# Optimization experiments

Hardware: AMD Instinct MI355X
Metric: run time of the kernel (lower is better)

## Reference

```python
import jax, jax.numpy as jnp
import numpy as np

NEG_SLOPE = 0.2  # PyG GATConv default leaky_relu slope
N_NODES, IN_DIM, HID, HEADS, OUT = 50000, 128, 64, 4, 128
N_EDGES = 800000


def gat_conv(x, src, dst, num_nodes, W, a_src, a_dst, bias, concat):
    """One PyG-style GATConv (add_self_loops already applied to src/dst)."""
    H, C = a_src.shape
    xp = (x @ W).reshape(num_nodes, H, C)            # (N,H,C)
    s = jnp.einsum('nhc,hc->nh', xp, a_src)          # per-node src score
    d = jnp.einsum('nhc,hc->nh', xp, a_dst)          # per-node dst score
    e = s[src] + d[dst]                              # (E,H)
    e = jnp.where(e > 0, e, NEG_SLOPE * e)           # leaky_relu
    # segment softmax over edges grouped by destination node
    m = jax.ops.segment_max(e, dst, num_segments=num_nodes)
    p = jnp.exp(e - m[dst])
    z = jax.ops.segment_sum(p, dst, num_segments=num_nodes)
    alpha = p / (z[dst] + 1e-16)                     # (E,H)
    # scatter-aggregate messages
    out = jax.ops.segment_sum(xp[src] * alpha[:, :, None], dst, num_segments=num_nodes)
    out = out.reshape(num_nodes, H * C) if concat else out.mean(axis=1)
    return out + bias


def setup_inputs() -> dict:
    key = jax.random.key(0)
    ks = jax.random.split(key, 16)
    HC = HEADS * HID
    inp = {
        'x': jax.random.normal(ks[0], (N_NODES, IN_DIM), dtype=jnp.float32),
        'edge_index': jax.random.randint(ks[1], (2, N_EDGES), 0, N_NODES, dtype=jnp.int32),
        'W0': jax.random.normal(ks[2], (IN_DIM, HC), dtype=jnp.float32) * 0.08,
        'a_src0': jax.random.normal(ks[3], (HEADS, HID), dtype=jnp.float32) * 0.1,
        'a_dst0': jax.random.normal(ks[4], (HEADS, HID), dtype=jnp.float32) * 0.1,
        'b0': jnp.zeros((HC,), dtype=jnp.float32),
        'W1': jax.random.normal(ks[5], (HC, HC), dtype=jnp.float32) * 0.06,
        'a_src1': jax.random.normal(ks[6], (HEADS, HID), dtype=jnp.float32) * 0.1,
        'a_dst1': jax.random.normal(ks[7], (HEADS, HID), dtype=jnp.float32) * 0.1,
        'b1': jnp.zeros((HC,), dtype=jnp.float32),
        'W2': jax.random.normal(ks[8], (HC, OUT), dtype=jnp.float32) * 0.06,
        'a_src2': jax.random.normal(ks[9], (1, OUT), dtype=jnp.float32) * 0.1,
        'a_dst2': jax.random.normal(ks[10], (1, OUT), dtype=jnp.float32) * 0.1,
        'b2': jnp.zeros((OUT,), dtype=jnp.float32),
    }
    return inp


def reference(x, edge_index, W0, a_src0, a_dst0, b0, W1, a_src1, a_dst1, b1, W2, a_src2, a_dst2, b2):
    N = x.shape[0]
    loops = jnp.arange(N, dtype=edge_index.dtype)  # add_self_loops=True
    src = jnp.concatenate([edge_index[0], loops])
    dst = jnp.concatenate([edge_index[1], loops])
    h = gat_conv(x, src, dst, N, W0, a_src0, a_dst0, b0, True)
    h = jax.nn.elu(h)
    h = gat_conv(h, src, dst, N, W1, a_src1, a_dst1, b1, True)
    h = jax.nn.elu(h)
    h = gat_conv(h, src, dst, N, W2, a_src2, a_dst2, b2, False)
    return h
```

## Files before the change

### kernel.cpp

```cpp
#include <hip/hip_runtime.h>
#include <hip/hip_bf16.h>
#include <hip/hip_fp16.h>
#include <math.h>

#define N_NODES 50000
#define N_EDGES 800000
#define ET      (N_EDGES + N_NODES)
#define IN_DIM  128
#define HEADS   4
#define HID     64
#define HC      256
#define OUTD    128

typedef _Float16 half8 __attribute__((ext_vector_type(8)));
typedef float f32x4 __attribute__((ext_vector_type(4)));


__global__ void scan1_k(const int* __restrict__ counts, int* __restrict__ offs,
                        int* __restrict__ bsums) {
    __shared__ int sm[512];
    int tid = threadIdx.x;
    int i = blockIdx.x * 512 + tid;
    int v = (i < N_NODES) ? counts[i] : 0;
    sm[tid] = v;
    __syncthreads();
    #pragma unroll
    for (int o = 1; o < 512; o <<= 1) {
        int add = (tid >= o) ? sm[tid - o] : 0;
        __syncthreads();
        sm[tid] += add;
        __syncthreads();
    }
    if (i < N_NODES) offs[i] = sm[tid] - v;
    if (tid == 511) bsums[blockIdx.x] = sm[511];
}

__global__ void scan3_k(int* __restrict__ offs, const int* __restrict__ bsums) {
    __shared__ int base_sm;
    int tid = threadIdx.x;
    if (tid < 64) {
        int p = 0;
        for (int j = tid; j < (int)blockIdx.x; j += 64) p += bsums[j];
        #pragma unroll
        for (int o = 1; o < 64; o <<= 1) p += __shfl_xor(p, o, 64);
        if (tid == 0) base_sm = p;
    }
    __syncthreads();
    int i = blockIdx.x * 512 + tid;
    if (i < N_NODES) offs[i] += base_sm;
    if (i == 0) offs[N_NODES] = ET;
}

__global__ void fill_k(const int* __restrict__ ei, const int* __restrict__ offs,
                       int* __restrict__ counts, int* __restrict__ csr) {
    int i = blockIdx.x * blockDim.x + threadIdx.x;
    if (i >= ET) return;
    int sv, dv;
    if (i < N_EDGES) { sv = ei[i]; dv = ei[N_EDGES + i]; }
    else             { sv = dv = i - N_EDGES; }
    int pos = offs[dv] + atomicSub(&counts[dv], 1) - 1;
    csr[pos] = sv;
}


#define J_HIST  ET
#define J_CVT   (N_NODES * IN_DIM / 4)
#define J_W     131072
#define SETUP_TOTAL (J_HIST + J_CVT + J_W + 2 * N_NODES)

__global__ void setup_k(const int* __restrict__ ei, int* __restrict__ counts,
                        const float* __restrict__ x, __half* __restrict__ xh,
                        const float* __restrict__ W0, __half* __restrict__ Wt0,
                        const float* __restrict__ W1, __half* __restrict__ Wt1,
                        const float* __restrict__ W2, __half* __restrict__ Wt2,
                        float* __restrict__ S2, float* __restrict__ D2) {
    int g = blockIdx.x * 256 + threadIdx.x;
    if (g < J_HIST) {
        int dv = (g < N_EDGES) ? ei[N_EDGES + g] : (g - N_EDGES);
        atomicAdd(&counts[dv], 1);
        return;
    }
    g -= J_HIST;
    if (g < J_CVT) {
        float4 v = *(const float4*)(x + (size_t)g * 4);
        union { __half2 h2[2]; float2 f2; } u;
        u.h2[0] = __floats2half2_rn(v.x, v.y);
        u.h2[1] = __floats2half2_rn(v.z, v.w);
        *(float2*)(xh + (size_t)g * 4) = u.f2;
        return;
    }
    g -= J_CVT;
    if (g < J_W) {
        if (g < 32768) {
            int n = g / IN_DIM, k = g - n * IN_DIM;
            Wt0[g] = __float2half(W0[(size_t)k * HC + n]);
        } else if (g < 98304) {
            int i = g - 32768;
            int n = i / HC, k = i - n * HC;
            Wt1[i] = __float2half(W1[(size_t)k * HC + n]);
        } else {
            int i = g - 98304;
            int n = i / HC, k = i - n * HC;
            Wt2[i] = __float2half(W2[(size_t)k * OUTD + n]);
        }
        return;
    }
    g -= J_W;
    if (g < N_NODES) { S2[g] = 0.f; return; }
    g -= N_NODES;
    if (g < N_NODES) D2[g] = 0.f;
}


__device__ __forceinline__ void async_copy16(void* lds_base, const void* gaddr) {
    __builtin_amdgcn_global_load_lds(
        (const __attribute__((address_space(1))) unsigned int*)gaddr,
        (__attribute__((address_space(3))) unsigned int*)lds_base,
        16, 0, 0);
}

#define CPAD 132

template<int H, int CD, bool ATOMIC>
__global__ __launch_bounds__(256) void gemm_mfma_k(const __half* __restrict__ A,
                                                   const __half* __restrict__ Wt,
                                                   __half* __restrict__ C,
                                                   const float* __restrict__ asrc,
                                                   const float* __restrict__ adst,
                                                   float* __restrict__ S,
                                                   float* __restrict__ D,
                                                   int M, int K, int N) {
    __shared__ __attribute__((aligned(16))) __half smem[128 * CPAD];
    __half* Ah = smem;
    __half* Bh = smem + 128 * 64;
    const int t = threadIdx.x;
    const int w = t >> 6;
    const int lane = t & 63;
    const int wm = w >> 1, wn = w & 1;
    const int cc = lane & 15;
    const int quad = lane >> 4;
    const int row0 = blockIdx.x * 128;
    const int col0 = blockIdx.y * 128;

    f32x4 acc[4][4];
    #pragma unroll
    for (int i = 0; i < 4; ++i)
        #pragma unroll
        for (int j = 0; j < 4; ++j) acc[i][j] = (f32x4){0.f, 0.f, 0.f, 0.f};

    const int srow = lane >> 3;
    const int skq  = (lane & 7) * 8;

    for (int k0 = 0; k0 < K; k0 += 64) {
        __syncthreads();
        #pragma unroll
        for (int hh = 0; hh < 4; ++hh) {
            int ra = row0 + w * 32 + hh * 8 + srow;
            if (ra > M - 1) ra = M - 1;
            async_copy16(&Ah[(w * 32 + hh * 8) * 64],
                         A + (size_t)ra * K + k0 + skq);
            int rb = col0 + w * 32 + hh * 8 + srow;
            async_copy16(&Bh[(w * 32 + hh * 8) * 64],
                         Wt + (size_t)rb * K + k0 + skq);
        }
        __syncthreads();
        #pragma unroll
        for (int c = 0; c < 2; ++c) {
            half8 a[4], b[4];
            #pragma unroll
            for (int i = 0; i < 4; ++i)
                a[i] = *(const half8*)&Ah[(wm * 64 + i * 16 + cc) * 64 + c * 32 + quad * 8];
            #pragma unroll
            for (int j = 0; j < 4; ++j)
                b[j] = *(const half8*)&Bh[(wn * 64 + j * 16 + cc) * 64 + c * 32 + quad * 8];
            #pragma unroll
            for (int i = 0; i < 4; ++i)
                #pragma unroll
                for (int j = 0; j < 4; ++j)
                    acc[i][j] = __builtin_amdgcn_mfma_f32_16x16x32_f16(b[j], a[i], acc[i][j], 0, 0, 0);
        }
    }

    const int hh_ = ATOMIC ? 0 : (blockIdx.y * 2 + wn);
    float4 asj[4], adj[4];
    #pragma unroll
    for (int j = 0; j < 4; ++j) {
        int cb = (ATOMIC ? wn * 64 : 0) + j * 16 + quad * 4;
        asj[j] = *(const float4*)&asrc[hh_ * CD + cb];
        adj[j] = *(const float4*)&adst[hh_ * CD + cb];
    }
    #pragma unroll
    for (int i = 0; i < 4; ++i) {
        float sv = 0.f, dv = 0.f;
        #pragma unroll
        for (int j = 0; j < 4; ++j) {
            sv = fmaf(acc[i][j][0], asj[j].x, sv); dv = fmaf(acc[i][j][0], adj[j].x, dv);
            sv = fmaf(acc[i][j][1], asj[j].y, sv); dv = fmaf(acc[i][j][1], adj[j].y, dv);
            sv = fmaf(acc[i][j][2], asj[j].z, sv); dv = fmaf(acc[i][j][2], adj[j].z, dv);
            sv = fmaf(acc[i][j][3], asj[j].w, sv); dv = fmaf(acc[i][j][3], adj[j].w, dv);
        }
        sv += __shfl_xor(sv, 16, 64); dv += __shfl_xor(dv, 16, 64);
        sv += __shfl_xor(sv, 32, 64); dv += __shfl_xor(dv, 32, 64);
        int r = row0 + wm * 64 + i * 16 + cc;
        if (quad == 0 && r < M) {
            if constexpr (ATOMIC) {
                atomicAdd(&S[r], sv);
                atomicAdd(&D[r], dv);
            } else {
                S[(size_t)r * H + hh_] = sv;
                D[(size_t)r * H + hh_] = dv;
            }
        }
    }

    __syncthreads();
    #pragma unroll
    for (int i = 0; i < 4; ++i) {
        int tr = wm * 64 + i * 16 + cc;
        #pragma unroll
        for (int j = 0; j < 4; ++j) {
            int tc = wn * 64 + j * 16 + quad * 4;
            union { __half2 h2[2]; uint2 u2; } pk;
            pk.h2[0] = __floats2half2_rn(acc[i][j][0], acc[i][j][1]);
            pk.h2[1] = __floats2half2_rn(acc[i][j][2], acc[i][j][3]);
            *(uint2*)&smem[tr * CPAD + tc] = pk.u2;
        }
    }
    __syncthreads();
    #pragma unroll
    for (int rr = 0; rr < 8; ++rr) {
        int r = rr * 16 + (t >> 4);
        int ccol = (t & 15) * 8;
        uint4 v = *(const uint4*)&smem[r * CPAD + ccol];
        int gr = row0 + r;
        if (gr < M)
            *(uint4*)&C[(size_t)gr * N + col0 + ccol] = v;
    }
}


template<int H, int C, bool ELU_OUT, typename OT>
__global__ __launch_bounds__(256) void aggr_k(const __half* __restrict__ xp,
                                              const float* __restrict__ s,
                                              const float* __restrict__ d,
                                              const int* __restrict__ offs,
                                              const int* __restrict__ csr,
                                              const float* __restrict__ bias,
                                              OT* __restrict__ out) {
    constexpr int HCl = H * C;
    constexpr int FPL = HCl / 32;
    constexpr int U = 8;
    const int tid = threadIdx.x;
    const int lane = tid & 63;
    const int l = lane & 31;
    const int par = lane >> 5;
    int wid = blockIdx.x * 4 + (tid >> 6);
    if (wid >= N_NODES) return;
    const int h = (l * FPL) / C;
    const int loff = l * FPL;

    float dh = d[wid * H + h];
    float z = 0.f;
    float acc[FPL];
    #pragma unroll
    for (int k = 0; k < FPL; ++k) acc[k] = 0.f;

    const int e0 = offs[wid];
    const int e1 = offs[wid + 1];

    for (int j = e0; j < e1; j += U) {
        int ss[4];
        #pragma unroll
        for (int k2 = 0; k2 < 4; ++k2) {
            int idx = j + 2 * k2 + par;
            ss[k2] = csr[idx < e1 ? idx : e1 - 1];
        }
        float ev[4];
        #pragma unroll
        for (int k2 = 0; k2 < 4; ++k2)
            ev[k2] = s[ss[k2] * H + h];
        uint4 r4[4];
        uint2 r2[4];
        #pragma unroll
        for (int k2 = 0; k2 < 4; ++k2) {
            const __half* rowp = xp + (size_t)ss[k2] * HCl + loff;
            if constexpr (FPL == 8) r4[k2] = *(const uint4*)rowp;
            else                    r2[k2] = *(const uint2*)rowp;
        }
        #pragma unroll
        for (int k2 = 0; k2 < 4; ++k2) {
            float e = (j + 2 * k2 + par < e1) ? (ev[k2] + dh) : -1e30f;
            e = fmaxf(e, 0.2f * e);
            float pw = __expf(e);
            z += pw;
            if constexpr (FPL == 8) {
                union { uint4 u; __half2 h2[4]; } rr; rr.u = r4[k2];
                #pragma unroll
                for (int q = 0; q < 4; ++q) {
                    acc[2*q]   = fmaf(pw, __half2float(__low2half(rr.h2[q])),  acc[2*q]);
                    acc[2*q+1] = fmaf(pw, __half2float(__high2half(rr.h2[q])), acc[2*q+1]);
                }
            } else {
                union { uint2 u; __half2 h2[2]; } rr; rr.u = r2[k2];
                #pragma unroll
                for (int q = 0; q < 2; ++q) {
                    acc[2*q]   = fmaf(pw, __half2float(__low2half(rr.h2[q])),  acc[2*q]);
                    acc[2*q+1] = fmaf(pw, __half2float(__high2half(rr.h2[q])), acc[2*q+1]);
                }
            }
        }
    }

    z += __shfl_xor(z, 32, 64);
    #pragma unroll
    for (int k = 0; k < FPL; ++k) acc[k] += __shfl_xor(acc[k], 32, 64);

    if (lane >= 32) return;

    float inv = 1.f / (z + 1e-16f);
    float o[FPL];
    #pragma unroll
    for (int k = 0; k < FPL; ++k) {
        o[k] = acc[k] * inv + bias[loff + k];
        if constexpr (ELU_OUT) o[k] = (o[k] > 0.f) ? o[k] : (__expf(o[k]) - 1.f);
    }
    if constexpr (sizeof(OT) == 2 && FPL == 8) {
        union { __half2 h2[4]; uint4 u4; } u;
        u.h2[0] = __floats2half2_rn(o[0], o[1]);
        u.h2[1] = __floats2half2_rn(o[2], o[3]);
        u.h2[2] = __floats2half2_rn(o[4], o[5]);
        u.h2[3] = __floats2half2_rn(o[6], o[7]);
        *(uint4*)((__half*)out + (size_t)wid * HCl + loff) = u.u4;
    } else if constexpr (sizeof(OT) == 4 && FPL == 4) {
        float4 v; v.x = o[0]; v.y = o[1]; v.z = o[2]; v.w = o[3];
        *(float4*)((float*)out + (size_t)wid * HCl + loff) = v;
    } else {
        #pragma unroll
        for (int k = 0; k < FPL; ++k)
            out[(size_t)wid * HCl + loff + k] = (OT)o[k];
    }
}


extern "C" void kernel_launch(void* const* d_in, const int* in_sizes, int n_in,
                              void* d_out, int out_size, void* d_ws, size_t ws_size,
                              hipStream_t stream) {
    const float* x      = (const float*)d_in[0];
    const int*   ei     = (const int*)  d_in[1];
    const float* W0     = (const float*)d_in[2];
    const float* as0    = (const float*)d_in[3];
    const float* ad0    = (const float*)d_in[4];
    const float* b0     = (const float*)d_in[5];
    const float* W1     = (const float*)d_in[6];
    const float* as1    = (const float*)d_in[7];
    const float* ad1    = (const float*)d_in[8];
    const float* b1     = (const float*)d_in[9];
    const float* W2     = (const float*)d_in[10];
    const float* as2    = (const float*)d_in[11];
    const float* ad2    = (const float*)d_in[12];
    const float* b2     = (const float*)d_in[13];
    float* out = (float*)d_out;

    char* p = (char*)d_ws;
    auto take = [&](size_t bytes) {
        char* r = p;
        p += (bytes + 255) & ~(size_t)255;
        return r;
    };
    __half* XPh   = (__half*)take((size_t)N_NODES * HC * 2);
    __half* Hbuf  = (__half*)take((size_t)N_NODES * HC * 2);
    __half* xh    = (__half*)take((size_t)N_NODES * IN_DIM * 2);
    __half* Wt0   = (__half*)take((size_t)IN_DIM * HC * 2);
    __half* Wt1   = (__half*)take((size_t)HC * HC * 2);
    __half* Wt2   = (__half*)take((size_t)HC * OUTD * 2);
    float*  S     = (float*) take((size_t)N_NODES * HEADS * 4);
    float*  D     = (float*) take((size_t)N_NODES * HEADS * 4);
    float*  S2    = (float*) take((size_t)N_NODES * 4);
    float*  D2    = (float*) take((size_t)N_NODES * 4);
    int*    counts= (int*)   take((size_t)N_NODES * 4);
    int*    offs  = (int*)   take((size_t)(N_NODES + 1) * 4);
    int*    bsums = (int*)   take(512 * 4);
    int*    csr   = (int*)   take((size_t)ET * 4);

    const int NB_SCAN = (N_NODES + 511) / 512;
    const int ET_BLOCKS = (ET + 255) / 256;
    const int NODE_BLOCKS = (N_NODES + 3) / 4;
    const int MB = (N_NODES + 127) / 128;
    dim3 g0(MB, HC / 128);
    dim3 g2(MB, OUTD / 128);

    hipMemsetAsync(counts, 0, (size_t)N_NODES * 4, stream);
    setup_k<<<(SETUP_TOTAL + 255) / 256, 256, 0, stream>>>(
        ei, counts, x, xh, W0, Wt0, W1, Wt1, W2, Wt2, S2, D2);

    scan1_k<<<NB_SCAN, 512, 0, stream>>>(counts, offs, bsums);
    scan3_k<<<NB_SCAN, 512, 0, stream>>>(offs, bsums);
    fill_k<<<ET_BLOCKS, 256, 0, stream>>>(ei, offs, counts, csr);

    gemm_mfma_k<HEADS, HID, false><<<g0, 256, 0, stream>>>(xh, Wt0, XPh, as0, ad0, S, D, N_NODES, IN_DIM, HC);
    aggr_k<HEADS, HID, true, __half><<<NODE_BLOCKS, 256, 0, stream>>>(XPh, S, D, offs, csr, b0, Hbuf);

    gemm_mfma_k<HEADS, HID, false><<<g0, 256, 0, stream>>>(Hbuf, Wt1, XPh, as1, ad1, S, D, N_NODES, HC, HC);
    aggr_k<HEADS, HID, true, __half><<<NODE_BLOCKS, 256, 0, stream>>>(XPh, S, D, offs, csr, b1, Hbuf);

    gemm_mfma_k<1, OUTD, true><<<g2, 256, 0, stream>>>(Hbuf, Wt2, XPh, as2, ad2, S2, D2, N_NODES, HC, OUTD);
    aggr_k<1, OUTD, false, float><<<NODE_BLOCKS, 256, 0, stream>>>(XPh, S2, D2, offs, csr, b2, out);
}
```

Before: 388.8 us.

## Persistent double-buffered GEMM with direct B loads and 16-bit CSR indices

The MFMA GEMM becomes a persistent kernel. Each block loops over several M tiles and double-buffers A tiles in LDS, prefetching the next tile or K-chunk while computing the current one. B fragments are now read straight from global memory instead of being staged in LDS, and the output is written directly from registers rather than through an LDS transpose. The CSR neighbour array is narrowed to unsigned short to halve index traffic in the aggregation kernels, but node ids up to 49999 fit in 16 bits only because N is below 65536.

```diff
diff --git a/kernel.cpp b/kernel.cpp
--- a/kernel.cpp
+++ b/kernel.cpp
@@ -52,14 +52,14 @@
 }
 
 __global__ void fill_k(const int* __restrict__ ei, const int* __restrict__ offs,
-                       int* __restrict__ counts, int* __restrict__ csr) {
+                       int* __restrict__ counts, unsigned short* __restrict__ csr) {
     int i = blockIdx.x * blockDim.x + threadIdx.x;
     if (i >= ET) return;
     int sv, dv;
     if (i < N_EDGES) { sv = ei[i]; dv = ei[N_EDGES + i]; }
     else             { sv = dv = i - N_EDGES; }
     int pos = offs[dv] + atomicSub(&counts[dv], 1) - 1;
-    csr[pos] = sv;
+    csr[pos] = (unsigned short)sv;
 }
 
 
@@ -119,67 +119,40 @@
         16, 0, 0);
 }
 
-#define CPAD 132
-
-template<int H, int CD, bool ATOMIC>
-__global__ __launch_bounds__(256) void gemm_mfma_k(const __half* __restrict__ A,
-                                                   const __half* __restrict__ Wt,
-                                                   __half* __restrict__ C,
-                                                   const float* __restrict__ asrc,
-                                                   const float* __restrict__ adst,
-                                                   float* __restrict__ S,
-                                                   float* __restrict__ D,
-                                                   int M, int K, int N) {
-    __shared__ __attribute__((aligned(16))) __half smem[128 * CPAD];
-    __half* Ah = smem;
-    __half* Bh = smem + 128 * 64;
+template<int H, int CD, bool ATOMIC, int KK>
+__global__ __launch_bounds__(256, 3) void gemm_mfma_k(const __half* __restrict__ A,
+                                                      const __half* __restrict__ Wt,
+                                                      __half* __restrict__ C,
+                                                      const float* __restrict__ asrc,
+                                                      const float* __restrict__ adst,
+                                                      float* __restrict__ S,
+                                                      float* __restrict__ D,
+                                                      int M, int N) {
+    constexpr int KC = KK / 64;
+    __shared__ __attribute__((aligned(16))) __half Ah[2][128 * 64];
     const int t = threadIdx.x;
     const int w = t >> 6;
     const int lane = t & 63;
     const int wm = w >> 1, wn = w & 1;
     const int cc = lane & 15;
     const int quad = lane >> 4;
-    const int row0 = blockIdx.x * 128;
     const int col0 = blockIdx.y * 128;
-
-    f32x4 acc[4][4];
-    #pragma unroll
-    for (int i = 0; i < 4; ++i)
-        #pragma unroll
-        for (int j = 0; j < 4; ++j) acc[i][j] = (f32x4){0.f, 0.f, 0.f, 0.f};
-
     const int srow = lane >> 3;
     const int skq  = (lane & 7) * 8;
-
-    for (int k0 = 0; k0 < K; k0 += 64) {
-        __syncthreads();
+    const int MBt = (M + 127) >> 7;
+    const int PB = gridDim.x;
+
+    if ((int)blockIdx.x >= MBt) return;
+
+    auto stage = [&](int mt, int kc, int b) {
         #pragma unroll
         for (int hh = 0; hh < 4; ++hh) {
-            int ra = row0 + w * 32 + hh * 8 + srow;
+            int ra = mt * 128 + w * 32 + hh * 8 + srow;
             if (ra > M - 1) ra = M - 1;
-            async_copy16(&Ah[(w * 32 + hh * 8) * 64],
-                         A + (size_t)ra * K + k0 + skq);
-            int rb = col0 + w * 32 + hh * 8 + srow;
-            async_copy16(&Bh[(w * 32 + hh * 8) * 64],
-                         Wt + (size_t)rb * K + k0 + skq);
-        }
-        __syncthreads();
-        #pragma unroll
-        for (int c = 0; c < 2; ++c) {
-            half8 a[4], b[4];
-            #pragma unroll
-            for (int i = 0; i < 4; ++i)
-                a[i] = *(const half8*)&Ah[(wm * 64 + i * 16 + cc) * 64 + c * 32 + quad * 8];
-            #pragma unroll
-            for (int j = 0; j < 4; ++j)
-                b[j] = *(const half8*)&Bh[(wn * 64 + j * 16 + cc) * 64 + c * 32 + quad * 8];
-            #pragma unroll
-            for (int i = 0; i < 4; ++i)
-                #pragma unroll
-                for (int j = 0; j < 4; ++j)
-                    acc[i][j] = __builtin_amdgcn_mfma_f32_16x16x32_f16(b[j], a[i], acc[i][j], 0, 0, 0);
-        }
-    }
+            async_copy16(&Ah[b][(w * 32 + hh * 8) * 64],
+                         A + (size_t)ra * KK + kc * 64 + skq);
+        }
+    };
 
     const int hh_ = ATOMIC ? 0 : (blockIdx.y * 2 + wn);
     float4 asj[4], adj[4];
@@ -189,52 +162,85 @@
         asj[j] = *(const float4*)&asrc[hh_ * CD + cb];
         adj[j] = *(const float4*)&adst[hh_ * CD + cb];
     }
-    #pragma unroll
-    for (int i = 0; i < 4; ++i) {
-        float sv = 0.f, dv = 0.f;
-        #pragma unroll
-        for (int j = 0; j < 4; ++j) {
-            sv = fmaf(acc[i][j][0], asj[j].x, sv); dv = fmaf(acc[i][j][0], adj[j].x, dv);
-            sv = fmaf(acc[i][j][1], asj[j].y, sv); dv = fmaf(acc[i][j][1], adj[j].y, dv);
-            sv = fmaf(acc[i][j][2], asj[j].z, sv); dv = fmaf(acc[i][j][2], adj[j].z, dv);
-            sv = fmaf(acc[i][j][3], asj[j].w, sv); dv = fmaf(acc[i][j][3], adj[j].w, dv);
-        }
-        sv += __shfl_xor(sv, 16, 64); dv += __shfl_xor(dv, 16, 64);
-        sv += __shfl_xor(sv, 32, 64); dv += __shfl_xor(dv, 32, 64);
-        int r = row0 + wm * 64 + i * 16 + cc;
-        if (quad == 0 && r < M) {
-            if constexpr (ATOMIC) {
-                atomicAdd(&S[r], sv);
-                atomicAdd(&D[r], dv);
-            } else {
-                S[(size_t)r * H + hh_] = sv;
-                D[(size_t)r * H + hh_] = dv;
+
+    int buf = 0;
+    stage(blockIdx.x, 0, 0);
+    asm volatile("s_waitcnt vmcnt(0)" ::: "memory");
+    __builtin_amdgcn_s_barrier();
+
+    for (int mt = blockIdx.x; mt < MBt; mt += PB) {
+        f32x4 acc[4][4];
+        #pragma unroll
+        for (int i = 0; i < 4; ++i)
+            #pragma unroll
+            for (int j = 0; j < 4; ++j) acc[i][j] = (f32x4){0.f, 0.f, 0.f, 0.f};
+
+        #pragma unroll
+        for (int kc = 0; kc < KC; ++kc) {
+            int nmt = mt, nkc = kc + 1;
+            if (nkc == KC) { nmt = mt + PB; nkc = 0; }
+            if (nmt < MBt) stage(nmt, nkc, buf ^ 1);
+
+            #pragma unroll
+            for (int c = 0; c < 2; ++c) {
+                half8 a[4], b[4];
+                #pragma unroll
+                for (int j = 0; j < 4; ++j)
+                    b[j] = *(const half8*)&Wt[(size_t)(col0 + wn * 64 + j * 16 + cc) * KK
+                                              + kc * 64 + c * 32 + quad * 8];
+                #pragma unroll
+                for (int i = 0; i < 4; ++i)
+                    a[i] = *(const half8*)&Ah[buf][(wm * 64 + i * 16 + cc) * 64 + c * 32 + quad * 8];
+                #pragma unroll
+                for (int i = 0; i < 4; ++i)
+                    #pragma unroll
+                    for (int j = 0; j < 4; ++j)
+                        acc[i][j] = __builtin_amdgcn_mfma_f32_16x16x32_f16(b[j], a[i], acc[i][j], 0, 0, 0);
             }
-        }
-    }
-
-    __syncthreads();
-    #pragma unroll
-    for (int i = 0; i < 4; ++i) {
-        int tr = wm * 64 + i * 16 + cc;
-        #pragma unroll
-        for (int j = 0; j < 4; ++j) {
-            int tc = wn * 64 + j * 16 + quad * 4;
-            union { __half2 h2[2]; uint2 u2; } pk;
-            pk.h2[0] = __floats2half2_rn(acc[i][j][0], acc[i][j][1]);
-            pk.h2[1] = __floats2half2_rn(acc[i][j][2], acc[i][j][3]);
-            *(uint2*)&smem[tr * CPAD + tc] = pk.u2;
-        }
-    }
-    __syncthreads();
-    #pragma unroll
-    for (int rr = 0; rr < 8; ++rr) {
-        int r = rr * 16 + (t >> 4);
-        int ccol = (t & 15) * 8;
-        uint4 v = *(const uint4*)&smem[r * CPAD + ccol];
-        int gr = row0 + r;
-        if (gr < M)
-            *(uint4*)&C[(size_t)gr * N + col0 + ccol] = v;
+
+            asm volatile("s_waitcnt vmcnt(0)" ::: "memory");
+            __builtin_amdgcn_s_barrier();
+            __builtin_amdgcn_sched_barrier(0);
+            buf ^= 1;
+        }
+
+        #pragma unroll
+        for (int i = 0; i < 4; ++i) {
+            float sv = 0.f, dv = 0.f;
+            #pragma unroll
+            for (int j = 0; j < 4; ++j) {
+                sv = fmaf(acc[i][j][0], asj[j].x, sv); dv = fmaf(acc[i][j][0], adj[j].x, dv);
+                sv = fmaf(acc[i][j][1], asj[j].y, sv); dv = fmaf(acc[i][j][1], adj[j].y, dv);
+                sv = fmaf(acc[i][j][2], asj[j].z, sv); dv = fmaf(acc[i][j][2], adj[j].z, dv);
+                sv = fmaf(acc[i][j][3], asj[j].w, sv); dv = fmaf(acc[i][j][3], adj[j].w, dv);
+            }
+            sv += __shfl_xor(sv, 16, 64); dv += __shfl_xor(dv, 16, 64);
+            sv += __shfl_xor(sv, 32, 64); dv += __shfl_xor(dv, 32, 64);
+            int r = mt * 128 + wm * 64 + i * 16 + cc;
+            if (quad == 0 && r < M) {
+                if constexpr (ATOMIC) {
+                    atomicAdd(&S[r], sv);
+                    atomicAdd(&D[r], dv);
+                } else {
+                    S[(size_t)r * H + hh_] = sv;
+                    D[(size_t)r * H + hh_] = dv;
+                }
+            }
+        }
+
+        #pragma unroll
+        for (int i = 0; i < 4; ++i) {
+            int gr = mt * 128 + wm * 64 + i * 16 + cc;
+            if (gr >= M) continue;
+            #pragma unroll
+            for (int j = 0; j < 4; ++j) {
+                int tc = col0 + wn * 64 + j * 16 + quad * 4;
+                union { __half2 h2[2]; uint2 u2; } pk;
+                pk.h2[0] = __floats2half2_rn(acc[i][j][0], acc[i][j][1]);
+                pk.h2[1] = __floats2half2_rn(acc[i][j][2], acc[i][j][3]);
+                *(uint2*)&C[(size_t)gr * N + tc] = pk.u2;
+            }
+        }
     }
 }
 
@@ -244,7 +250,7 @@
                                               const float* __restrict__ s,
                                               const float* __restrict__ d,
                                               const int* __restrict__ offs,
-                                              const int* __restrict__ csr,
+                                              const unsigned short* __restrict__ csr,
                                               const float* __restrict__ bias,
                                               OT* __restrict__ out) {
     constexpr int HCl = H * C;
@@ -380,13 +386,13 @@
     int*    counts= (int*)   take((size_t)N_NODES * 4);
     int*    offs  = (int*)   take((size_t)(N_NODES + 1) * 4);
     int*    bsums = (int*)   take(512 * 4);
-    int*    csr   = (int*)   take((size_t)ET * 4);
+    unsigned short* csr = (unsigned short*)take((size_t)ET * 2);
 
     const int NB_SCAN = (N_NODES + 511) / 512;
     const int ET_BLOCKS = (ET + 255) / 256;
     const int NODE_BLOCKS = (N_NODES + 3) / 4;
     const int MB = (N_NODES + 127) / 128;
-    dim3 g0(MB, HC / 128);
+    dim3 g0(MB < 384 ? MB : 384, HC / 128);
     dim3 g2(MB, OUTD / 128);
 
     hipMemsetAsync(counts, 0, (size_t)N_NODES * 4, stream);
@@ -397,12 +403,12 @@
     scan3_k<<<NB_SCAN, 512, 0, stream>>>(offs, bsums);
     fill_k<<<ET_BLOCKS, 256, 0, stream>>>(ei, offs, counts, csr);
 
-    gemm_mfma_k<HEADS, HID, false><<<g0, 256, 0, stream>>>(xh, Wt0, XPh, as0, ad0, S, D, N_NODES, IN_DIM, HC);
+    gemm_mfma_k<HEADS, HID, false, IN_DIM><<<g0, 256, 0, stream>>>(xh, Wt0, XPh, as0, ad0, S, D, N_NODES, HC);
     aggr_k<HEADS, HID, true, __half><<<NODE_BLOCKS, 256, 0, stream>>>(XPh, S, D, offs, csr, b0, Hbuf);
 
-    gemm_mfma_k<HEADS, HID, false><<<g0, 256, 0, stream>>>(Hbuf, Wt1, XPh, as1, ad1, S, D, N_NODES, HC, HC);
+    gemm_mfma_k<HEADS, HID, false, HC><<<g0, 256, 0, stream>>>(Hbuf, Wt1, XPh, as1, ad1, S, D, N_NODES, HC);
     aggr_k<HEADS, HID, true, __half><<<NODE_BLOCKS, 256, 0, stream>>>(XPh, S, D, offs, csr, b1, Hbuf);
 
-    gemm_mfma_k<1, OUTD, true><<<g2, 256, 0, stream>>>(Hbuf, Wt2, XPh, as2, ad2, S2, D2, N_NODES, HC, OUTD);
+    gemm_mfma_k<1, OUTD, true, HC><<<g2, 256, 0, stream>>>(Hbuf, Wt2, XPh, as2, ad2, S2, D2, N_NODES, OUTD);
     aggr_k<1, OUTD, false, float><<<NODE_BLOCKS, 256, 0, stream>>>(XPh, S2, D2, offs, csr, b2, out);
 }
```

Result: slower. 425.6 us (+9.5%).

## Fuse CSR scan and fill into one kernel with in-kernel spin-wait barrier

Applied to the files above, without the earlier changes.

Merges the two scan kernels and the fill kernel into a single launch. Scan blocks publish their partial sums through flagged atomics, and all blocks spin on a completion counter before scattering edges via an atomic cursor. CSR source indices are stored as 16-bit values, which fits because node ids stay below 65536, halving index bandwidth in the aggregation kernels. The GEMM epilogue now writes its output straight to global memory instead of staging it in LDS. The spin-wait relies on the 98 scan blocks being resident before waiting blocks occupy the GPU, which risks deadlock or stalls, and the direct 8-byte stores are less coalesced.

```diff
diff --git a/kernel.cpp b/kernel.cpp
--- a/kernel.cpp
+++ b/kernel.cpp
@@ -11,56 +11,10 @@
 #define HID     64
 #define HC      256
 #define OUTD    128
+#define NB_SCAN 98
 
 typedef _Float16 half8 __attribute__((ext_vector_type(8)));
 typedef float f32x4 __attribute__((ext_vector_type(4)));
-
-
-__global__ void scan1_k(const int* __restrict__ counts, int* __restrict__ offs,
-                        int* __restrict__ bsums) {
-    __shared__ int sm[512];
-    int tid = threadIdx.x;
-    int i = blockIdx.x * 512 + tid;
-    int v = (i < N_NODES) ? counts[i] : 0;
-    sm[tid] = v;
-    __syncthreads();
-    #pragma unroll
-    for (int o = 1; o < 512; o <<= 1) {
-        int add = (tid >= o) ? sm[tid - o] : 0;
-        __syncthreads();
-        sm[tid] += add;
-        __syncthreads();
-    }
-    if (i < N_NODES) offs[i] = sm[tid] - v;
-    if (tid == 511) bsums[blockIdx.x] = sm[511];
-}
-
-__global__ void scan3_k(int* __restrict__ offs, const int* __restrict__ bsums) {
-    __shared__ int base_sm;
-    int tid = threadIdx.x;
-    if (tid < 64) {
-        int p = 0;
-        for (int j = tid; j < (int)blockIdx.x; j += 64) p += bsums[j];
-        #pragma unroll
-        for (int o = 1; o < 64; o <<= 1) p += __shfl_xor(p, o, 64);
-        if (tid == 0) base_sm = p;
-    }
-    __syncthreads();
-    int i = blockIdx.x * 512 + tid;
-    if (i < N_NODES) offs[i] += base_sm;
-    if (i == 0) offs[N_NODES] = ET;
-}
-
-__global__ void fill_k(const int* __restrict__ ei, const int* __restrict__ offs,
-                       int* __restrict__ counts, int* __restrict__ csr) {
-    int i = blockIdx.x * blockDim.x + threadIdx.x;
-    if (i >= ET) return;
-    int sv, dv;
-    if (i < N_EDGES) { sv = ei[i]; dv = ei[N_EDGES + i]; }
-    else             { sv = dv = i - N_EDGES; }
-    int pos = offs[dv] + atomicSub(&counts[dv], 1) - 1;
-    csr[pos] = sv;
-}
 
 
 #define J_HIST  ET
@@ -112,14 +66,72 @@
 }
 
 
+__global__ void csr_k(const int* __restrict__ ei, const int* __restrict__ counts,
+                      int* __restrict__ offs, int* __restrict__ cursor,
+                      int* __restrict__ bsums, int* __restrict__ scan_done,
+                      unsigned short* __restrict__ csr) {
+    __shared__ int sm[512];
+    __shared__ int base_sm;
+    const int tid = threadIdx.x;
+
+    if ((int)blockIdx.x < NB_SCAN) {
+        int i = blockIdx.x * 512 + tid;
+        int v = (i < N_NODES) ? counts[i] : 0;
+        sm[tid] = v;
+        __syncthreads();
+        #pragma unroll
+        for (int o = 1; o < 512; o <<= 1) {
+            int add = (tid >= o) ? sm[tid - o] : 0;
+            __syncthreads();
+            sm[tid] += add;
+            __syncthreads();
+        }
+        if (tid == 511) atomicExch(&bsums[blockIdx.x], sm[511] + 1);
+        if (tid < 64) {
+            int p = 0;
+            for (int j = tid; j < (int)blockIdx.x; j += 64) {
+                int v2;
+                do { v2 = atomicAdd(&bsums[j], 0); } while (v2 == 0);
+                p += v2 - 1;
+            }
+            #pragma unroll
+            for (int o = 1; o < 64; o <<= 1) p += __shfl_xor(p, o, 64);
+            if (tid == 0) base_sm = p;
+        }
+        __syncthreads();
+        if (i < N_NODES) {
+            int off = base_sm + sm[tid] - v;
+            offs[i] = off;
+            atomicExch(&cursor[i], off);
+        }
+        if (i == 0) offs[N_NODES] = ET;
+        __threadfence();
+        __syncthreads();
+        if (tid == 0) atomicAdd(scan_done, 1);
+    }
+
+    if (tid == 0) {
+        while (atomicAdd(scan_done, 0) < NB_SCAN) __builtin_amdgcn_s_sleep(8);
+    }
+    __syncthreads();
+    __threadfence();
+    int i = blockIdx.x * 512 + tid;
+    if (i < ET) {
+        int sv, dv;
+        if (i < N_EDGES) { sv = ei[i]; dv = ei[N_EDGES + i]; }
+        else             { sv = dv = i - N_EDGES; }
+        int pos = atomicAdd(&cursor[dv], 1);
+        csr[pos] = (unsigned short)sv;
+    }
+}
+
+
 __device__ __forceinline__ void async_copy16(void* lds_base, const void* gaddr) {
     __builtin_amdgcn_global_load_lds(
         (const __attribute__((address_space(1))) unsigned int*)gaddr,
         (__attribute__((address_space(3))) unsigned int*)lds_base,
         16, 0, 0);
 }
-
-#define CPAD 132
 
 template<int H, int CD, bool ATOMIC>
 __global__ __launch_bounds__(256) void gemm_mfma_k(const __half* __restrict__ A,
@@ -130,7 +142,7 @@
                                                    float* __restrict__ S,
                                                    float* __restrict__ D,
                                                    int M, int K, int N) {
-    __shared__ __attribute__((aligned(16))) __half smem[128 * CPAD];
+    __shared__ __attribute__((aligned(16))) __half smem[2 * 128 * 64];
     __half* Ah = smem;
     __half* Bh = smem + 128 * 64;
     const int t = threadIdx.x;
@@ -213,28 +225,18 @@
         }
     }
 
-    __syncthreads();
     #pragma unroll
     for (int i = 0; i < 4; ++i) {
-        int tr = wm * 64 + i * 16 + cc;
+        int gr = row0 + wm * 64 + i * 16 + cc;
+        if (gr >= M) continue;
         #pragma unroll
         for (int j = 0; j < 4; ++j) {
-            int tc = wn * 64 + j * 16 + quad * 4;
+            int tc = col0 + wn * 64 + j * 16 + quad * 4;
             union { __half2 h2[2]; uint2 u2; } pk;
             pk.h2[0] = __floats2half2_rn(acc[i][j][0], acc[i][j][1]);
             pk.h2[1] = __floats2half2_rn(acc[i][j][2], acc[i][j][3]);
-            *(uint2*)&smem[tr * CPAD + tc] = pk.u2;
-        }
-    }
-    __syncthreads();
-    #pragma unroll
-    for (int rr = 0; rr < 8; ++rr) {
-        int r = rr * 16 + (t >> 4);
-        int ccol = (t & 15) * 8;
-        uint4 v = *(const uint4*)&smem[r * CPAD + ccol];
-        int gr = row0 + r;
-        if (gr < M)
-            *(uint4*)&C[(size_t)gr * N + col0 + ccol] = v;
+            *(uint2*)&C[(size_t)gr * N + tc] = pk.u2;
+        }
     }
 }
 
@@ -244,7 +246,7 @@
                                               const float* __restrict__ s,
                                               const float* __restrict__ d,
                                               const int* __restrict__ offs,
-                                              const int* __restrict__ csr,
+                                              const unsigned short* __restrict__ csr,
                                               const float* __restrict__ bias,
                                               OT* __restrict__ out) {
     constexpr int HCl = H * C;
@@ -377,25 +379,25 @@
     float*  D     = (float*) take((size_t)N_NODES * HEADS * 4);
     float*  S2    = (float*) take((size_t)N_NODES * 4);
     float*  D2    = (float*) take((size_t)N_NODES * 4);
-    int*    counts= (int*)   take((size_t)N_NODES * 4);
+    int*    zblob = (int*)   take((size_t)(N_NODES + 128 + 16) * 4);
+    int*    counts    = zblob;
+    int*    bsums     = zblob + N_NODES;
+    int*    scan_done = zblob + N_NODES + 128;
     int*    offs  = (int*)   take((size_t)(N_NODES + 1) * 4);
-    int*    bsums = (int*)   take(512 * 4);
-    int*    csr   = (int*)   take((size_t)ET * 4);
-
-    const int NB_SCAN = (N_NODES + 511) / 512;
-    const int ET_BLOCKS = (ET + 255) / 256;
+    int*    cursor= (int*)   take((size_t)N_NODES * 4);
+    unsigned short* csr = (unsigned short*)take((size_t)ET * 2);
+
+    const int ET_BLOCKS512 = (ET + 511) / 512;
     const int NODE_BLOCKS = (N_NODES + 3) / 4;
     const int MB = (N_NODES + 127) / 128;
     dim3 g0(MB, HC / 128);
     dim3 g2(MB, OUTD / 128);
 
-    hipMemsetAsync(counts, 0, (size_t)N_NODES * 4, stream);
+    hipMemsetAsync(zblob, 0, (size_t)(N_NODES + 128 + 16) * 4, stream);
     setup_k<<<(SETUP_TOTAL + 255) / 256, 256, 0, stream>>>(
         ei, counts, x, xh, W0, Wt0, W1, Wt1, W2, Wt2, S2, D2);
 
-    scan1_k<<<NB_SCAN, 512, 0, stream>>>(counts, offs, bsums);
-    scan3_k<<<NB_SCAN, 512, 0, stream>>>(offs, bsums);
-    fill_k<<<ET_BLOCKS, 256, 0, stream>>>(ei, offs, counts, csr);
+    csr_k<<<ET_BLOCKS512, 512, 0, stream>>>(ei, counts, offs, cursor, bsums, scan_done, csr);
 
     gemm_mfma_k<HEADS, HID, false><<<g0, 256, 0, stream>>>(xh, Wt0, XPh, as0, ad0, S, D, N_NODES, IN_DIM, HC);
     aggr_k<HEADS, HID, true, __half><<<NODE_BLOCKS, 256, 0, stream>>>(XPh, S, D, offs, csr, b0, Hbuf);
```

Measured after the change: 643.6 us. 1.66x slower.
